# Performance work log

Measured on AMD Instinct MI355X. Metric: run time of the kernel, lower is better.

Reference implementation:

```python
import jax, jax.numpy as jnp
import numpy as np

B, S, D, H, L, V, FFM = 4, 2048, 512, 8, 6, 8000, 4
HD = D // H
FF = FFM * D


def setup_inputs() -> dict:
    key = jax.random.key(0)
    ks = jax.random.split(key, 12)
    sc = 0.02
    return {
        "tokens": jax.random.randint(ks[0], (B, S), 0, V),
        "embed": jax.random.normal(ks[1], (V, D), jnp.float32) * sc,
        "wq": jax.random.normal(ks[2], (L, D, D), jnp.float32) * sc,
        "wk": jax.random.normal(ks[3], (L, D, D), jnp.float32) * sc,
        "wv": jax.random.normal(ks[4], (L, D, D), jnp.float32) * sc,
        "wo": jax.random.normal(ks[5], (L, D, D), jnp.float32) * sc,
        "bo": jnp.zeros((L, D), jnp.float32),
        "w1": jax.random.normal(ks[6], (L, D, FF), jnp.float32) * sc,
        "b1": jnp.zeros((L, FF), jnp.float32),
        "w2": jax.random.normal(ks[7], (L, FF, D), jnp.float32) * sc,
        "b2": jnp.zeros((L, D), jnp.float32),
        "ln_g": jnp.ones((L, D), jnp.float32),
        "ln_b": jnp.zeros((L, D), jnp.float32),
        "lnf_g": jnp.ones((D,), jnp.float32),
        "lnf_b": jnp.zeros((D,), jnp.float32),
        "w_out": jax.random.normal(ks[8], (D, V), jnp.float32) * sc,
        "b_out": jnp.zeros((V,), jnp.float32),
    }


def _layernorm(x, g, b, eps=1e-5):
    m = jnp.mean(x, -1, keepdims=True)
    v = jnp.var(x, -1, keepdims=True)
    return (x - m) * jax.lax.rsqrt(v + eps) * g + b


def _pos_encoding():
    pos = jnp.arange(S, dtype=jnp.float32)[:, None]
    div = jnp.exp(jnp.arange(0, D, 2, dtype=jnp.float32) * (-np.log(10000.0) / D))
    pe = jnp.zeros((S, D), jnp.float32)
    pe = pe.at[:, 0::2].set(jnp.sin(pos * div))
    pe = pe.at[:, 1::2].set(jnp.cos(pos * div))
    return pe


def _forward(tokens, embed, wq, wk, wv, wo, bo, w1, b1, w2, b2, ln_g, ln_b,
             lnf_g, lnf_b, w_out, b_out):
    x = embed[tokens] + _pos_encoding()[None]  # [B,S,D]
    causal = jnp.tril(jnp.ones((S, S), bool))
    neg_inf = jnp.float32(-jnp.inf)
    # NOTE: original scales scores by 1/sqrt(n_embd) (key.weight.size(-1) == D)
    inv_scale = 1.0 / jnp.sqrt(jnp.float32(D))

    def block(x, p):
        pwq, pwk, pwv, pwo, pbo, pw1, pb1, pw2, pb2, g, b = p
        # attention sublayer (same LayerNorm params used for both sublayers,
        # matching the repo's reuse of add_and_norm_1)
        h = _layernorm(x, g, b)
        q = (h @ pwq).reshape(B, S, H, HD)
        k = (h @ pwk).reshape(B, S, H, HD)
        v = (h @ pwv).reshape(B, S, H, HD)
        scores = jnp.einsum('bqhd,bkhd->bhqk', q, k) * inv_scale
        scores = jnp.where(causal, scores, neg_inf)
        att = jax.nn.softmax(scores, axis=-1)
        o = jnp.einsum('bhqk,bkhd->bqhd', att, v).reshape(B, S, D)
        x = x + o @ pwo + pbo
        # FFN sublayer
        h2 = _layernorm(x, g, b)
        x = x + jax.nn.relu(h2 @ pw1 + pb1) @ pw2 + pb2
        return x, None

    params = (wq, wk, wv, wo, bo, w1, b1, w2, b2, ln_g, ln_b)
    x, _ = jax.lax.scan(block, x, params)
    x = _layernorm(x, lnf_g, lnf_b)
    logits = x @ w_out + b_out  # [B,S,V]
    return logits


def reference(tokens, embed, wq, wk, wv, wo, bo, w1, b1, w2, b2, ln_g, ln_b,
              lnf_g, lnf_b, w_out, b_out):
    return _forward(tokens, embed, wq, wk, wv, wo, bo, w1, b1, w2, b2,
                    ln_g, ln_b, lnf_g, lnf_b, w_out, b_out)
```

## Files before the change

### kernel.cpp

```cpp
#include <hip/hip_runtime.h>

#define Bsz 4
#define Ssz 2048
#define Dsz 512
#define Hsz 8
#define Lsz 6
#define Vsz 8000
#define FFsz 2048
#define Msz (Bsz*Ssz)
#define VszPad 8192

typedef unsigned short u16;
typedef unsigned int u32;
typedef __attribute__((ext_vector_type(8))) short bf16x8;
typedef __attribute__((ext_vector_type(4))) float f32x4;
typedef __attribute__((ext_vector_type(16))) float f32x16;
typedef __attribute__((ext_vector_type(4))) u32 u32x4;

__device__ __forceinline__ u16 f2b(float f) {
    union { float f; unsigned u; } x; x.f = f;
    return (u16)((x.u + 0x7fffu + ((x.u >> 16) & 1u)) >> 16);
}
__device__ __forceinline__ float b2f(u16 v) {
    union { u32 u; float f; } x; x.u = ((u32)v) << 16; return x.f;
}

#define GLOAD_LDS16(g, l) __builtin_amdgcn_global_load_lds( \
    (const __attribute__((address_space(1))) u32*)(g), \
    (__attribute__((address_space(3))) u32*)(l), 16, 0, 0)

__global__ __launch_bounds__(256) void embed_kernel(const int* __restrict__ tokens,
                                                    const float* __restrict__ embed,
                                                    u16* __restrict__ x) {
    int idx = blockIdx.x * 256 + threadIdx.x;
    int row = idx >> 8, p = idx & 255;
    int tok = tokens[row];
    int s = row & (Ssz - 1);
    float div = __expf((float)p * (-9.210340371976184f / 256.f));
    float ang = (float)s * div;
    float2 e = ((const float2*)(embed + (size_t)tok * Dsz))[p];
    u32 o = (u32)f2b(e.x + sinf(ang)) | ((u32)f2b(e.y + cosf(ang)) << 16);
    ((u32*)(x + (size_t)row * Dsz))[p] = o;
}

__global__ __launch_bounds__(256) void ln_kernel(const u16* __restrict__ x,
                                                 const float* __restrict__ g,
                                                 const float* __restrict__ bta,
                                                 u16* __restrict__ out) {
    int wave = threadIdx.x >> 6, lane = threadIdx.x & 63;
    int row = blockIdx.x * 4 + wave;
    bf16x8 a = ((const bf16x8*)(x + (size_t)row * Dsz))[lane];
    float vals[8];
    #pragma unroll
    for (int i = 0; i < 8; ++i) vals[i] = b2f((u16)a[i]);
    float s = 0.f;
    #pragma unroll
    for (int i = 0; i < 8; ++i) s += vals[i];
    #pragma unroll
    for (int o = 32; o; o >>= 1) s += __shfl_xor(s, o);
    float mean = s * (1.f / 512.f);
    float sq = 0.f;
    #pragma unroll
    for (int i = 0; i < 8; ++i) { float d = vals[i] - mean; sq += d * d; }
    #pragma unroll
    for (int o = 32; o; o >>= 1) sq += __shfl_xor(sq, o);
    float rstd = rsqrtf(sq * (1.f / 512.f) + 1e-5f);
    int base = lane * 8;
    bf16x8 rv;
    #pragma unroll
    for (int i = 0; i < 8; ++i)
        rv[i] = (short)f2b((vals[i] - mean) * rstd * g[base + i] + bta[base + i]);
    *(bf16x8*)(out + (size_t)row * Dsz + base) = rv;
}

__global__ __launch_bounds__(256) void tconv_kernel(const float* __restrict__ src,
                                                    u16* __restrict__ dst,
                                                    int R, int C,
                                                    size_t sstride, size_t dstride) {
    __shared__ float tile[32][33];
    const float* s = src + blockIdx.z * sstride;
    u16* d = dst + blockIdx.z * dstride;
    int c0 = blockIdx.x * 32, r0 = blockIdx.y * 32;
    int tx = threadIdx.x & 31, ty = threadIdx.x >> 5;
    #pragma unroll
    for (int i = 0; i < 32; i += 8)
        tile[ty + i][tx] = s[(size_t)(r0 + ty + i) * C + c0 + tx];
    __syncthreads();
    #pragma unroll
    for (int i = 0; i < 32; i += 8)
        d[(size_t)(c0 + ty + i) * R + r0 + tx] = f2b(tile[tx][ty + i]);
}

__global__ __launch_bounds__(256) void vtrans_kernel(const u16* __restrict__ qkv,
                                                     u16* __restrict__ vT) {
    __shared__ u16 tile[32][33];
    int bh = blockIdx.z, b = bh >> 3, hh = bh & 7;
    int s0 = blockIdx.x * 32, d0 = blockIdx.y * 32;
    int tx = threadIdx.x & 31, ty = threadIdx.x >> 5;
    #pragma unroll
    for (int i = 0; i < 32; i += 8)
        tile[ty + i][tx] = qkv[(size_t)(b * Ssz + s0 + ty + i) * 1536 + 1024 + hh * 64 + d0 + tx];
    __syncthreads();
    #pragma unroll
    for (int i = 0; i < 32; i += 8)
        vT[((size_t)bh * 64 + d0 + ty + i) * Ssz + s0 + tx] = tile[tx][ty + i];
}

template<bool BIAS, bool RES, bool RELU, bool OF32, bool OBF16, bool XN, int BMF>
__global__ __launch_bounds__(256, 4) void gemm_kernel(const u16* __restrict__ A,
                                                   const u16* __restrict__ BT,
                                                   const float* __restrict__ bias,
                                                   const u16* __restrict__ res,
                                                   float* __restrict__ outf,
                                                   u16* __restrict__ outb,
                                                   int M, int N, int K) {
    __shared__ u16 As[BMF * 32 * 64];
    __shared__ u16 Bs[128 * 64];
    int tid = threadIdx.x;
    int wave = tid >> 6, lane = tid & 63;
    int wm = wave >> 1, wn = wave & 1;
    int gx = gridDim.x;
    int bid = blockIdx.y * gx + blockIdx.x;
    int xcd = bid & 7, j = bid >> 3;
    int mblk, nblk;
    if (XN) { mblk = j >> 3; nblk = xcd * 8 + (j & 7); }
    else    { int sm = gridDim.y >> 3; mblk = xcd * sm + j / gx; nblk = j % gx; }
    int m0 = mblk * (BMF * 32), n0 = nblk * 128;
    int lr = lane & 15, lg = lane >> 4;
    int srow = lane >> 3;
    int scol = (lane & 7) * 8;
    f32x4 acc[BMF][4] = {};
    for (int k0 = 0; k0 < K; k0 += 64) {
        #pragma unroll
        for (int i = 0; i < BMF; ++i) {
            int chunk = wave * BMF + i;
            int r = chunk * 8 + srow;
            GLOAD_LDS16(A + (size_t)(m0 + r) * K + k0 + scol, &As[chunk * 512]);
        }
        #pragma unroll
        for (int i = 0; i < 4; ++i) {
            int chunk = wave * 4 + i;
            int r = chunk * 8 + srow;
            GLOAD_LDS16(BT + (size_t)(n0 + r) * K + k0 + scol, &Bs[chunk * 512]);
        }
        __syncthreads();
        #pragma unroll
        for (int kk = 0; kk < 2; ++kk) {
            bf16x8 af[BMF], bfr[4];
            #pragma unroll
            for (int m = 0; m < BMF; ++m)
                af[m] = *(const bf16x8*)(As + (wm * (BMF * 16) + m * 16 + lr) * 64 + kk * 32 + lg * 8);
            #pragma unroll
            for (int n = 0; n < 4; ++n)
                bfr[n] = *(const bf16x8*)(Bs + (wn * 64 + n * 16 + lr) * 64 + kk * 32 + lg * 8);
            #pragma unroll
            for (int m = 0; m < BMF; ++m)
                #pragma unroll
                for (int n = 0; n < 4; ++n)
                    acc[m][n] = __builtin_amdgcn_mfma_f32_16x16x32_bf16(af[m], bfr[n], acc[m][n], 0, 0, 0);
        }
        __syncthreads();
    }
    #pragma unroll
    for (int m = 0; m < BMF; ++m) {
        int row = m0 + wm * (BMF * 16) + m * 16 + lg * 4;
        #pragma unroll
        for (int n = 0; n < 4; ++n) {
            int col = n0 + wn * 64 + n * 16 + lr;
            if (col < N) {
                float bv = BIAS ? bias[col] : 0.f;
                #pragma unroll
                for (int j2 = 0; j2 < 4; ++j2) {
                    float v = acc[m][n][j2] + bv;
                    if (RES) v += b2f(res[(size_t)(row + j2) * N + col]);
                    if (RELU) v = fmaxf(v, 0.f);
                    if (OF32) outf[(size_t)(row + j2) * N + col] = v;
                    if (OBF16) outb[(size_t)(row + j2) * N + col] = f2b(v);
                }
            }
        }
    }
}

__global__ __launch_bounds__(256, 2) void flash5_kernel(const u16* __restrict__ qkv,
                                                        const u16* __restrict__ vT,
                                                        u16* __restrict__ o) {
    __shared__ u16 Ks[2][64 * 64];
    __shared__ u16 Vs[2][64 * 64];
    int blk = blockIdx.x;
    int bh = blk & 31;
    int c = 15 - (blk >> 5);
    int b = bh >> 3, hh = bh & 7;
    int tid = threadIdx.x, wave = tid >> 6, lane = tid & 63;
    int l31 = lane & 31, h5 = lane >> 5;
    int g = c * 4 + wave;
    int qg = g * 32 + l31;
    int ext = (g >> 1) + 1;
    int nt = 2 * c + 2;
    const float cs = 0.044194173824159216f;

    bf16x8 qf[4];
    {
        const u16* qrow = qkv + (size_t)(b * Ssz + qg) * 1536 + hh * 64;
        #pragma unroll
        for (int cb = 0; cb < 4; ++cb)
            qf[cb] = *(const bf16x8*)(qrow + cb * 16 + h5 * 8);
    }
    f32x16 Oa0 = {}, Oa1 = {};
    float m_run = -1e30f, l_run = 0.f;
    int sr = tid >> 3;
    int sc2 = (tid & 7) * 8;
    const u16* kbase = qkv + (size_t)(b * Ssz) * 1536 + 512 + hh * 64;
    const u16* vbase = vT + (size_t)bh * 64 * Ssz;
    int byteA = (sr * 128 + sc2 * 2) ^ ((sr & 7) << 4);
    int byteB = ((sr + 32) * 128 + sc2 * 2) ^ ((sr & 7) << 4);

    {
        bf16x8 kA = *(const bf16x8*)(kbase + (size_t)sr * 1536 + sc2);
        bf16x8 kB = *(const bf16x8*)(kbase + (size_t)(32 + sr) * 1536 + sc2);
        bf16x8 vA = *(const bf16x8*)(vbase + (size_t)sr * Ssz + sc2);
        bf16x8 vB = *(const bf16x8*)(vbase + (size_t)(32 + sr) * Ssz + sc2);
        *(bf16x8*)((char*)Ks[0] + byteA) = kA;
        *(bf16x8*)((char*)Ks[0] + byteB) = kB;
        *(bf16x8*)((char*)Vs[0] + byteA) = vA;
        *(bf16x8*)((char*)Vs[0] + byteB) = vB;
    }
    __syncthreads();

    for (int kt = 0; kt < nt; ++kt) {
        int cur = kt & 1;
        bool pf = (kt + 1 < nt);
        bf16x8 kA, kB, vA, vB;
        if (pf) {
            kA = *(const bf16x8*)(kbase + (size_t)((kt + 1) * 64 + sr) * 1536 + sc2);
            kB = *(const bf16x8*)(kbase + (size_t)((kt + 1) * 64 + 32 + sr) * 1536 + sc2);
            vA = *(const bf16x8*)(vbase + (size_t)sr * Ssz + (kt + 1) * 64 + sc2);
            vB = *(const bf16x8*)(vbase + (size_t)(32 + sr) * Ssz + (kt + 1) * 64 + sc2);
        }
        const u16* Kc = Ks[cur];
        const u16* Vc = Vs[cur];
        if (kt < ext) {
            bool dtile = (kt == ext - 1);
            int mts = (dtile && !(g & 1)) ? 1 : 2;
            f32x16 st[2] = {};
            __builtin_amdgcn_s_setprio(1);
            #pragma unroll
            for (int mt = 0; mt < 2; ++mt)
                if (mt < mts) {
                    int r = mt * 32 + l31;
                    #pragma unroll
                    for (int cb = 0; cb < 4; ++cb) {
                        int byte = (r * 128 + (cb * 16 + h5 * 8) * 2) ^ ((r & 7) << 4);
                        bf16x8 kf = *(const bf16x8*)((char*)Kc + byte);
                        st[mt] = __builtin_amdgcn_mfma_f32_32x32x16_bf16(kf, qf[cb], st[mt], 0, 0, 0);
                    }
                }
            __builtin_amdgcn_s_setprio(0);
            float pmax = -1e30f;
            #pragma unroll
            for (int mt = 0; mt < 2; ++mt)
                if (mt < mts)
                    #pragma unroll
                    for (int r = 0; r < 16; ++r) {
                        float v = st[mt][r];
                        if (dtile) {
                            int kglob = kt * 64 + mt * 32 + (r & 3) + 8 * (r >> 2) + 4 * h5;
                            if (kglob > qg) v = -1e30f;
                        }
                        st[mt][r] = v;
                        pmax = fmaxf(pmax, v);
                    }
            pmax = fmaxf(pmax, __shfl_xor(pmax, 32));
            if (!__all(pmax - m_run <= 181.019336f)) {
                float mn = fmaxf(m_run, pmax);
                float al = __expf((m_run - mn) * cs);
                l_run *= al;
                #pragma unroll
                for (int r = 0; r < 16; ++r) {
                    int qloc = (r & 3) + 8 * (r >> 2) + 4 * h5;
                    float alr = __shfl(al, qloc);
                    Oa0[r] *= alr; Oa1[r] *= alr;
                }
                m_run = mn;
            }
            float ls = 0.f;
            u32 pk[2][8];
            #pragma unroll
            for (int mt = 0; mt < 2; ++mt)
                if (mt < mts)
                    #pragma unroll
                    for (int w = 0; w < 8; ++w) {
                        float p0 = __expf((st[mt][2 * w]     - m_run) * cs);
                        float p1 = __expf((st[mt][2 * w + 1] - m_run) * cs);
                        ls += p0 + p1;
                        pk[mt][w] = (u32)f2b(p0) | ((u32)f2b(p1) << 16);
                    }
            l_run += ls + __shfl_xor(ls, 32);
            __builtin_amdgcn_s_setprio(1);
            #pragma unroll
            for (int mt = 0; mt < 2; ++mt)
                if (mt < mts) {
                    u32 pko[8];
                    #pragma unroll
                    for (int w = 0; w < 8; ++w)
                        pko[w] = __shfl_xor(pk[mt][w], 32);
                    #pragma unroll
                    for (int kbl = 0; kbl < 2; ++kbl) {
                        int kb = mt * 2 + kbl;
                        u32x4 aw;
                        #pragma unroll
                        for (int w = 0; w < 4; ++w) {
                            int widx = 4 * kbl + 2 * h5 + (w & 1);
                            bool own = (w < 2) != (h5 == 1);
                            aw[w] = own ? pk[mt][widx] : pko[widx];
                        }
                        bf16x8 af = __builtin_bit_cast(bf16x8, aw);
                        #pragma unroll
                        for (int dt = 0; dt < 2; ++dt) {
                            int r = dt * 32 + l31;
                            int byte = (r * 128 + (kb * 16 + h5 * 8) * 2) ^ ((r & 7) << 4);
                            bf16x8 vf = *(const bf16x8*)((char*)Vc + byte);
                            if (dt == 0) Oa0 = __builtin_amdgcn_mfma_f32_32x32x16_bf16(af, vf, Oa0, 0, 0, 0);
                            else         Oa1 = __builtin_amdgcn_mfma_f32_32x32x16_bf16(af, vf, Oa1, 0, 0, 0);
                        }
                    }
                }
            __builtin_amdgcn_s_setprio(0);
        }
        if (pf) {
            u16* Kn = Ks[cur ^ 1];
            u16* Vn = Vs[cur ^ 1];
            *(bf16x8*)((char*)Kn + byteA) = kA;
            *(bf16x8*)((char*)Kn + byteB) = kB;
            *(bf16x8*)((char*)Vn + byteA) = vA;
            *(bf16x8*)((char*)Vn + byteB) = vB;
        }
        __syncthreads();
    }
    float rln = 1.f / l_run;
    u16* obase = o + (size_t)(b * Ssz) * Dsz + hh * 64;
    #pragma unroll
    for (int r = 0; r < 16; ++r) {
        int qloc = (r & 3) + 8 * (r >> 2) + 4 * h5;
        float s = __shfl(rln, qloc);
        u16* orow = obase + (size_t)(g * 32 + qloc) * Dsz + l31;
        orow[0]  = f2b(Oa0[r] * s);
        orow[32] = f2b(Oa1[r] * s);
    }
}

extern "C" void kernel_launch(void* const* d_in, const int* in_sizes, int n_in,
                              void* d_out, int out_size, void* d_ws, size_t ws_size,
                              hipStream_t stream) {
    (void)in_sizes; (void)n_in; (void)out_size; (void)ws_size;
    const int*   tokens = (const int*)d_in[0];
    const float* embed  = (const float*)d_in[1];
    const float* wq     = (const float*)d_in[2];
    const float* wk     = (const float*)d_in[3];
    const float* wv     = (const float*)d_in[4];
    const float* wo     = (const float*)d_in[5];
    const float* bo     = (const float*)d_in[6];
    const float* w1     = (const float*)d_in[7];
    const float* b1     = (const float*)d_in[8];
    const float* w2     = (const float*)d_in[9];
    const float* b2     = (const float*)d_in[10];
    const float* ln_g   = (const float*)d_in[11];
    const float* ln_b   = (const float*)d_in[12];
    const float* lnf_g  = (const float*)d_in[13];
    const float* lnf_b  = (const float*)d_in[14];
    const float* w_out  = (const float*)d_in[15];
    const float* b_out  = (const float*)d_in[16];
    float* out = (float*)d_out;

    char* ws = (char*)d_ws;
    size_t off = 0;
    auto alloc = [&](size_t bytes) {
        void* p = ws + off;
        off += (bytes + 255) & ~(size_t)255;
        return p;
    };
    u16*   x     = (u16*)alloc((size_t)Msz * Dsz * 2);
    u16*   h     = (u16*)alloc((size_t)Msz * Dsz * 2);
    u16*   qkv   = (u16*)alloc((size_t)Msz * 1536 * 2);
    u16*   vT    = (u16*)alloc((size_t)Bsz * Hsz * 64 * Ssz * 2);
    u16*   ob    = (u16*)alloc((size_t)Msz * Dsz * 2);
    u16*   ffh   = (u16*)alloc((size_t)Msz * FFsz * 2);
    u16*   wqkvT = (u16*)alloc((size_t)Lsz * 3 * Dsz * Dsz * 2);
    u16*   woT   = (u16*)alloc((size_t)Lsz * Dsz * Dsz * 2);
    u16*   w1T   = (u16*)alloc((size_t)Lsz * FFsz * Dsz * 2);
    u16*   w2T   = (u16*)alloc((size_t)Lsz * Dsz * FFsz * 2);
    u16*   w_outT= (u16*)alloc((size_t)VszPad * Dsz * 2);

    dim3 tb(256);
    size_t dd = (size_t)Dsz * Dsz;
    hipMemsetAsync(w_outT + (size_t)Vsz * Dsz, 0, (size_t)(VszPad - Vsz) * Dsz * 2, stream);
    tconv_kernel<<<dim3(16, 16, Lsz), tb, 0, stream>>>(wq, wqkvT + 0 * dd, Dsz, Dsz, dd, 3 * dd);
    tconv_kernel<<<dim3(16, 16, Lsz), tb, 0, stream>>>(wk, wqkvT + 1 * dd, Dsz, Dsz, dd, 3 * dd);
    tconv_kernel<<<dim3(16, 16, Lsz), tb, 0, stream>>>(wv, wqkvT + 2 * dd, Dsz, Dsz, dd, 3 * dd);
    tconv_kernel<<<dim3(16, 16, Lsz), tb, 0, stream>>>(wo, woT, Dsz, Dsz, dd, dd);
    tconv_kernel<<<dim3(64, 16, Lsz), tb, 0, stream>>>(w1, w1T, Dsz, FFsz, (size_t)Dsz * FFsz, (size_t)FFsz * Dsz);
    tconv_kernel<<<dim3(16, 64, Lsz), tb, 0, stream>>>(w2, w2T, FFsz, Dsz, (size_t)FFsz * Dsz, (size_t)Dsz * FFsz);
    tconv_kernel<<<dim3(250, 16, 1), tb, 0, stream>>>(w_out, w_outT, Dsz, Vsz, 0, 0);

    embed_kernel<<<Msz * 256 / 256, tb, 0, stream>>>(tokens, embed, x);

    for (int l = 0; l < Lsz; ++l) {
        ln_kernel<<<Msz / 4, tb, 0, stream>>>(x, ln_g + l * Dsz, ln_b + l * Dsz, h);
        gemm_kernel<false, false, false, false, true, false, 4><<<dim3(12, Msz / 128), tb, 0, stream>>>(
            h, wqkvT + (size_t)l * 3 * dd, nullptr, nullptr, nullptr, qkv, Msz, 1536, Dsz);
        vtrans_kernel<<<dim3(Ssz / 32, 2, Bsz * Hsz), tb, 0, stream>>>(qkv, vT);
        flash5_kernel<<<dim3(512), tb, 0, stream>>>(qkv, vT, ob);
        gemm_kernel<true, true, false, false, true, false, 2><<<dim3(4, Msz / 64), tb, 0, stream>>>(
            ob, woT + (size_t)l * dd, bo + l * Dsz, x, nullptr, x, Msz, Dsz, Dsz);
        ln_kernel<<<Msz / 4, tb, 0, stream>>>(x, ln_g + l * Dsz, ln_b + l * Dsz, h);
        gemm_kernel<true, false, true, false, true, false, 4><<<dim3(16, Msz / 128), tb, 0, stream>>>(
            h, w1T + (size_t)l * FFsz * Dsz, b1 + l * FFsz, nullptr, nullptr, ffh, Msz, FFsz, Dsz);
        gemm_kernel<true, true, false, false, true, false, 2><<<dim3(4, Msz / 64), tb, 0, stream>>>(
            ffh, w2T + (size_t)l * Dsz * FFsz, b2 + l * Dsz, x, nullptr, x, Msz, Dsz, FFsz);
    }
    ln_kernel<<<Msz / 4, tb, 0, stream>>>(x, lnf_g, lnf_b, h);
    gemm_kernel<true, false, false, true, false, true, 4><<<dim3(64, Msz / 128), tb, 0, stream>>>(
        h, w_outT, b_out, nullptr, out, nullptr, Msz, Vsz, Dsz);
}
```

Baseline: 1.569 ms.

## Add 256x256-tile GEMM kernel and fuse V transpose into QKV epilogue

```diff
diff --git a/kernel.cpp b/kernel.cpp
--- a/kernel.cpp
+++ b/kernel.cpp
@@ -16,6 +16,7 @@
 typedef __attribute__((ext_vector_type(4))) float f32x4;
 typedef __attribute__((ext_vector_type(16))) float f32x16;
 typedef __attribute__((ext_vector_type(4))) u32 u32x4;
+typedef __attribute__((ext_vector_type(4))) u16 u16x4;
 
 __device__ __forceinline__ u16 f2b(float f) {
     union { float f; unsigned u; } x; x.f = f;
@@ -89,21 +90,6 @@
     #pragma unroll
     for (int i = 0; i < 32; i += 8)
         d[(size_t)(c0 + ty + i) * R + r0 + tx] = f2b(tile[tx][ty + i]);
-}
-
-__global__ __launch_bounds__(256) void vtrans_kernel(const u16* __restrict__ qkv,
-                                                     u16* __restrict__ vT) {
-    __shared__ u16 tile[32][33];
-    int bh = blockIdx.z, b = bh >> 3, hh = bh & 7;
-    int s0 = blockIdx.x * 32, d0 = blockIdx.y * 32;
-    int tx = threadIdx.x & 31, ty = threadIdx.x >> 5;
-    #pragma unroll
-    for (int i = 0; i < 32; i += 8)
-        tile[ty + i][tx] = qkv[(size_t)(b * Ssz + s0 + ty + i) * 1536 + 1024 + hh * 64 + d0 + tx];
-    __syncthreads();
-    #pragma unroll
-    for (int i = 0; i < 32; i += 8)
-        vT[((size_t)bh * 64 + d0 + ty + i) * Ssz + s0 + tx] = tile[tx][ty + i];
 }
 
 template<bool BIAS, bool RES, bool RELU, bool OF32, bool OBF16, bool XN, int BMF>
@@ -173,6 +159,84 @@
                 for (int j2 = 0; j2 < 4; ++j2) {
                     float v = acc[m][n][j2] + bv;
                     if (RES) v += b2f(res[(size_t)(row + j2) * N + col]);
+                    if (RELU) v = fmaxf(v, 0.f);
+                    if (OF32) outf[(size_t)(row + j2) * N + col] = v;
+                    if (OBF16) outb[(size_t)(row + j2) * N + col] = f2b(v);
+                }
+            }
+        }
+    }
+}
+
+template<bool BIAS, bool RELU, bool OF32, bool OBF16, int MAP, bool QKV>
+__global__ __launch_bounds__(512, 2) void gemm256_kernel(const u16* __restrict__ A,
+                                                         const u16* __restrict__ BT,
+                                                         const float* __restrict__ bias,
+                                                         float* __restrict__ outf,
+                                                         u16* __restrict__ outb,
+                                                         u16* __restrict__ vT,
+                                                         int M, int N, int K) {
+    __shared__ u16 As[256 * 64];
+    __shared__ u16 Bs[256 * 64];
+    int tid = threadIdx.x;
+    int wid = tid >> 6, lane = tid & 63;
+    int wr = wid >> 2, wc = wid & 3;
+    int lr = lane & 15, lg = lane >> 4;
+    int bid = blockIdx.y * gridDim.x + blockIdx.x;
+    int xcd = bid & 7, j = bid >> 3;
+    int mblk, nblk;
+    if (MAP == 0) { int npx = gridDim.x >> 3; if (npx < 1) npx = 1;
+                    nblk = xcd * npx + j % npx; mblk = j / npx; }
+    else          { int mpx = gridDim.y >> 3;
+                    mblk = xcd * mpx + j / gridDim.x; nblk = j % gridDim.x; }
+    int m0 = mblk * 256, n0 = nblk * 256;
+    int grow = tid >> 3;
+    int gcol = (tid & 7) * 8;
+    f32x4 acc[8][4] = {};
+    for (int k0 = 0; k0 < K; k0 += 64) {
+        #pragma unroll
+        for (int i = 0; i < 4; ++i) {
+            int r = i * 64 + grow;
+            GLOAD_LDS16(A + (size_t)(m0 + r) * K + k0 + gcol, &As[(i * 64 + wid * 8) * 64]);
+            GLOAD_LDS16(BT + (size_t)(n0 + r) * K + k0 + gcol, &Bs[(i * 64 + wid * 8) * 64]);
+        }
+        __syncthreads();
+        #pragma unroll
+        for (int kk = 0; kk < 2; ++kk) {
+            bf16x8 af[8], bfr[4];
+            #pragma unroll
+            for (int m = 0; m < 8; ++m)
+                af[m] = *(const bf16x8*)(As + (wr * 128 + m * 16 + lr) * 64 + kk * 32 + lg * 8);
+            #pragma unroll
+            for (int n = 0; n < 4; ++n)
+                bfr[n] = *(const bf16x8*)(Bs + (wc * 64 + n * 16 + lr) * 64 + kk * 32 + lg * 8);
+            #pragma unroll
+            for (int m = 0; m < 8; ++m)
+                #pragma unroll
+                for (int n = 0; n < 4; ++n)
+                    acc[m][n] = __builtin_amdgcn_mfma_f32_16x16x32_bf16(af[m], bfr[n], acc[m][n], 0, 0, 0);
+        }
+        __syncthreads();
+    }
+    #pragma unroll
+    for (int m = 0; m < 8; ++m) {
+        int row = m0 + wr * 128 + m * 16 + lg * 4;
+        #pragma unroll
+        for (int n = 0; n < 4; ++n) {
+            int col = n0 + wc * 64 + n * 16 + lr;
+            if (QKV && col >= 1024) {
+                int hd = col - 1024;
+                int hh = hd >> 6; hd &= 63;
+                int b = row >> 11, s = row & 2047;
+                u16x4 v4;
+                #pragma unroll
+                for (int j2 = 0; j2 < 4; ++j2) v4[j2] = f2b(acc[m][n][j2]);
+                *(u16x4*)(vT + ((size_t)(b * 8 + hh) * 64 + hd) * Ssz + s) = v4;
+            } else if (col < N) {
+                float bv = BIAS ? bias[col] : 0.f;
+                #pragma unroll
+                for (int j2 = 0; j2 < 4; ++j2) {
+                    float v = acc[m][n][j2] + bv;
                     if (RELU) v = fmaxf(v, 0.f);
                     if (OF32) outf[(size_t)(row + j2) * N + col] = v;
                     if (OBF16) outb[(size_t)(row + j2) * N + col] = f2b(v);
@@ -406,19 +470,18 @@
 
     for (int l = 0; l < Lsz; ++l) {
         ln_kernel<<<Msz / 4, tb, 0, stream>>>(x, ln_g + l * Dsz, ln_b + l * Dsz, h);
-        gemm_kernel<false, false, false, false, true, false, 4><<<dim3(12, Msz / 128), tb, 0, stream>>>(
-            h, wqkvT + (size_t)l * 3 * dd, nullptr, nullptr, nullptr, qkv, Msz, 1536, Dsz);
-        vtrans_kernel<<<dim3(Ssz / 32, 2, Bsz * Hsz), tb, 0, stream>>>(qkv, vT);
+        gemm256_kernel<false, false, false, true, 1, true><<<dim3(6, Msz / 256), dim3(512), 0, stream>>>(
+            h, wqkvT + (size_t)l * 3 * dd, nullptr, nullptr, qkv, vT, Msz, 1536, Dsz);
         flash5_kernel<<<dim3(512), tb, 0, stream>>>(qkv, vT, ob);
         gemm_kernel<true, true, false, false, true, false, 2><<<dim3(4, Msz / 64), tb, 0, stream>>>(
             ob, woT + (size_t)l * dd, bo + l * Dsz, x, nullptr, x, Msz, Dsz, Dsz);
         ln_kernel<<<Msz / 4, tb, 0, stream>>>(x, ln_g + l * Dsz, ln_b + l * Dsz, h);
-        gemm_kernel<true, false, true, false, true, false, 4><<<dim3(16, Msz / 128), tb, 0, stream>>>(
-            h, w1T + (size_t)l * FFsz * Dsz, b1 + l * FFsz, nullptr, nullptr, ffh, Msz, FFsz, Dsz);
+        gemm256_kernel<true, true, false, true, 0, false><<<dim3(FFsz / 256, Msz / 256), dim3(512), 0, stream>>>(
+            h, w1T + (size_t)l * FFsz * Dsz, b1 + l * FFsz, nullptr, ffh, nullptr, Msz, FFsz, Dsz);
         gemm_kernel<true, true, false, false, true, false, 2><<<dim3(4, Msz / 64), tb, 0, stream>>>(
             ffh, w2T + (size_t)l * Dsz * FFsz, b2 + l * Dsz, x, nullptr, x, Msz, Dsz, FFsz);
     }
     ln_kernel<<<Msz / 4, tb, 0, stream>>>(x, lnf_g, lnf_b, h);
-    gemm_kernel<true, false, false, true, false, true, 4><<<dim3(64, Msz / 128), tb, 0, stream>>>(
-        h, w_outT, b_out, nullptr, out, nullptr, Msz, Vsz, Dsz);
-}
+    gemm256_kernel<true, false, true, false, 0, false><<<dim3(VszPad / 256, Msz / 256), dim3(512), 0, stream>>>(
+        h, w_outT, b_out, out, nullptr, nullptr, Msz, Vsz, Dsz);
+}
```

Result: slower. 1.690 ms (+7.8%).
